# Kernel optimization log

Measured on AMD Instinct MI355X. Metric: run time of the kernel, lower is better.

The kernel has to match this reference:

```python
import jax, jax.numpy as jnp
import numpy as np

RATIOS = (0.5, 1.0, 2.0)
SCALES = (8.0, 16.0, 32.0)
BASE = 7.0
FEAT = 16
N_PRE = 6000    # pre-NMS top-k (test-mode default of standard ProposalCreator)
N_POST = 300    # post-NMS proposals per image (fixed -> jit-safe padded output)
NMS_T = 0.7
MIN_SIZE = 16.0
SCALE = 1.0     # forward arg `scale` default
NA = 9          # len(ratios)*len(anchor_scales)


def anchor_base():
    ab = np.zeros((NA, 4), np.float32)
    for i, r in enumerate(RATIOS):
        for j, s in enumerate(SCALES):
            h = BASE * s * np.sqrt(r)
            w = BASE * s * np.sqrt(1.0 / r)
            k = i * len(SCALES) + j
            ab[k] = [BASE / 2 - h / 2, BASE / 2 - w / 2, BASE / 2 + h / 2, BASE / 2 + w / 2]
    return jnp.asarray(ab)


def enum_anchors(H, W):
    # positions-major ordering: (H*W, 9, 4) -> (H*W*9, 4), matching permute(0,2,3,1)
    ab = anchor_base()
    sy = jnp.arange(H, dtype=jnp.float32) * FEAT
    sx = jnp.arange(W, dtype=jnp.float32) * FEAT
    ys, xs = jnp.meshgrid(sy, sx, indexing='ij')
    shift = jnp.stack([ys.ravel(), xs.ravel(), ys.ravel(), xs.ravel()], axis=1)
    return (shift[:, None, :] + ab[None, :, :]).reshape(-1, 4)


def conv2d(x, w, b, pad):
    y = jax.lax.conv_general_dilated(x, w, (1, 1), pad,
                                     dimension_numbers=('NCHW', 'OIHW', 'NCHW'))
    return y + b[None, :, None, None]


def decode(anchors, loc):
    ah = anchors[:, 2] - anchors[:, 0]
    aw = anchors[:, 3] - anchors[:, 1]
    acy = anchors[:, 0] + 0.5 * ah
    acx = anchors[:, 1] + 0.5 * aw
    dy, dx, dh, dw = loc[:, 0], loc[:, 1], loc[:, 2], loc[:, 3]
    cy = dy * ah + acy
    cx = dx * aw + acx
    h = jnp.exp(dh) * ah
    w = jnp.exp(dw) * aw
    return jnp.stack([cy - 0.5 * h, cx - 0.5 * w, cy + 0.5 * h, cx + 0.5 * w], axis=1)


def iou_matrix(b):
    tl = jnp.maximum(b[:, None, :2], b[None, :, :2])
    br = jnp.minimum(b[:, None, 2:], b[None, :, 2:])
    inter = jnp.prod(jnp.clip(br - tl, 0.0, None), axis=-1)
    area = jnp.prod(b[:, 2:] - b[:, :2], axis=-1)
    return inter / (area[:, None] + area[None, :] - inter + 1e-9)


def propose(loc, fg, anchors, img_h, img_w):
    boxes = decode(anchors, loc)
    boxes = jnp.stack([jnp.clip(boxes[:, 0], 0.0, img_h),
                       jnp.clip(boxes[:, 1], 0.0, img_w),
                       jnp.clip(boxes[:, 2], 0.0, img_h),
                       jnp.clip(boxes[:, 3], 0.0, img_w)], axis=1)
    hs = boxes[:, 2] - boxes[:, 0]
    ws = boxes[:, 3] - boxes[:, 1]
    ms = MIN_SIZE * SCALE
    valid = (hs >= ms) & (ws >= ms)
    score = jnp.where(valid, fg, -jnp.inf)
    _, idx = jax.lax.top_k(score, N_PRE)          # sorted by score desc
    bk = boxes[idx]                                # [N_PRE, 4]
    iou = iou_matrix(bk)                           # [N_PRE, N_PRE]

    def body(suppr, xs):
        row, i = xs
        keep_i = jnp.logical_not(suppr[i])
        suppr = suppr | (keep_i & (row > NMS_T) & (jnp.arange(N_PRE) > i))
        return suppr, None

    suppr, _ = jax.lax.scan(body, jnp.zeros(N_PRE, bool), (iou, jnp.arange(N_PRE)))
    keep = jnp.logical_not(suppr)
    # kept boxes first (already score-ordered), padded with trailing boxes
    sel = jnp.argsort(jnp.where(keep, jnp.arange(N_PRE), N_PRE))[:N_POST]
    return bk[sel]


def setup_inputs():
    key = jax.random.key(0)
    ks = jax.random.split(key, 4)
    N, C, H, W = 8, 256, 64, 64
    mid = 256
    return {
        'x': jax.random.normal(ks[0], (N, C, H, W), jnp.float32),
        'conv1_w': jax.random.normal(ks[1], (mid, C, 3, 3), jnp.float32) * 0.02,
        'conv1_b': jnp.zeros((mid,), jnp.float32),
        'score_w': jax.random.normal(ks[2], (NA * 2, mid, 1, 1), jnp.float32) * 0.02,
        'score_b': jnp.zeros((NA * 2,), jnp.float32),
        'loc_w': jax.random.normal(ks[3], (NA * 4, mid, 1, 1), jnp.float32) * 0.02,
        'loc_b': jnp.zeros((NA * 4,), jnp.float32),
        'img_h': 1024,
        'img_w': 1024,
    }


def reference(x, conv1_w, conv1_b, score_w, score_b, loc_w, loc_b, img_h, img_w):
    N, _, H, W = x.shape
    h = jax.nn.relu(conv2d(x, conv1_w, conv1_b, 'SAME'))
    rpn_loc = conv2d(h, loc_w, loc_b, 'VALID')
    rpn_score = conv2d(h, score_w, score_b, 'VALID')
    anchors = enum_anchors(H, W)                                 # [H*W*9, 4]
    rpn_loc = rpn_loc.transpose(0, 2, 3, 1).reshape(N, -1, 4)    # [N, A, 4]
    rpn_score = rpn_score.transpose(0, 2, 3, 1)                  # [N, H, W, 18]
    sm = jax.nn.softmax(rpn_score.reshape(N, H, W, NA, 2), axis=-1)
    fg = sm[..., 1].reshape(N, -1)                               # [N, A]
    rpn_score = rpn_score.reshape(N, -1, 2)
    fh, fw = float(img_h), float(img_w)
    rois = jax.lax.map(lambda a: propose(a[0], a[1], anchors, fh, fw),
                       (rpn_loc, fg)).reshape(-1, 4)             # [N*N_POST, 4]
    roi_indices = jnp.repeat(jnp.arange(N), N_POST)
    return rpn_loc, rpn_score, rois, roi_indices, anchors
```

## Files before the change

kernel.cpp:

```cpp
#include <hip/hip_runtime.h>
#include <cstdint>
#include <cstddef>

#define NBATCH 8
#define MID 256
#define HIMG 64
#define WIMG 64
#define NA 9
#define NPRE 6000
#define NPOST 300
#define NANCH (HIMG*WIMG*NA)
#define NWORDS 94
#define GCOLS 6016
#define LOROWS 16

#define OUT_LOC   0
#define OUT_SCORE 1179648
#define OUT_ROIS  1769472
#define OUT_RIDX  1779072
#define OUT_ANCH  1781472

#define H_OFF    0ul
#define H_BYTES  (8ul*256*64*64*4)
#define WT_OFF   (H_OFF + H_BYTES)
#define WT_BYTES (2304ul*256*4)
#define BOX_OFF  (WT_OFF + WT_BYTES)
#define BOX_BYTES (8ul*36864*4*4)
#define U_OFF    (BOX_OFF + BOX_BYTES)
#define U_BYTES  (8ul*36864*4)
#define CK_OFF   (U_OFF + U_BYTES)
#define CK_BYTES (8ul*8192*8)
#define CC_OFF   (CK_OFF + CK_BYTES)
#define CC_BYTES 64ul
#define BK_OFF   (CC_OFF + CC_BYTES)
#define BK_BYTES (8ul*6000*16)
#define M_OFF    (BK_OFF + BK_BYTES + 64)
#define M_BYTES  (8ul*NWORDS*GCOLS*8)

typedef _Float16 f16x8 __attribute__((ext_vector_type(8)));
typedef _Float16 f16x4 __attribute__((ext_vector_type(4)));
typedef float f32x16 __attribute__((ext_vector_type(16)));

__global__ __launch_bounds__(256) void k_prep_w(const float* __restrict__ w,
                                                const float* __restrict__ loc_w,
                                                const float* __restrict__ score_w,
                                                _Float16* __restrict__ w3h,
                                                _Float16* __restrict__ w3l,
                                                _Float16* __restrict__ whh,
                                                _Float16* __restrict__ whl,
                                                float* __restrict__ out,
                                                unsigned int* __restrict__ cc) {
    int idx = blockIdx.x * 256 + threadIdx.x;
    if (idx < 16) cc[idx] = 0u;
    if (idx < 589824) {
        int e  = idx & 7;
        int t  = idx >> 3;
        int oc = t & 255; t >>= 8;
        int g  = t & 1;   t >>= 1;
        int kb = t & 15;  t >>= 4;
        int s  = t;
        int ic = kb * 16 + g * 8 + e;
        float v = w[(oc * 256 + ic) * 9 + s] * 64.0f;
        _Float16 vh = (_Float16)v;
        w3h[idx] = vh;
        w3l[idx] = (_Float16)(v - (float)vh);
    } else if (idx < 589824 + 16384) {
        int j = idx - 589824;
        int e  = j & 7;
        int c  = (j >> 3) & 63;
        int g  = (j >> 9) & 1;
        int kb = j >> 10;
        int k  = kb * 16 + g * 8 + e;
        float v = (c < 36) ? loc_w[c * 256 + k]
                 : ((c < 54) ? score_w[(c - 36) * 256 + k] : 0.0f);
        v *= 64.0f;
        _Float16 vh = (_Float16)v;
        whh[j] = vh;
        whl[j] = (_Float16)(v - (float)vh);
    }
    if (idx < NANCH) {
        int p = idx / 9, a = idx - p * 9;
        int y = p >> 6, xg = p & 63;
        double rr = (a < 3) ? 0.5 : ((a < 6) ? 1.0 : 2.0);
        int sj = a % 3;
        double ssc = (sj == 0) ? 8.0 : ((sj == 1) ? 16.0 : 32.0);
        double hh = 7.0 * ssc * sqrt(rr);
        double ww = 7.0 * ssc * sqrt(1.0 / rr);
        float a0 = (float)(3.5 - 0.5 * hh), a2 = (float)(3.5 + 0.5 * hh);
        float b0 = (float)(3.5 - 0.5 * ww), b2 = (float)(3.5 + 0.5 * ww);
        float* dst = out + OUT_ANCH + (size_t)idx * 4;
        dst[0] = y * 16.0f + a0;
        dst[1] = xg * 16.0f + b0;
        dst[2] = y * 16.0f + a2;
        dst[3] = xg * 16.0f + b2;
    }
}

__global__ __launch_bounds__(1024) void k_conv1m(const float* __restrict__ x,
                                                 const _Float16* __restrict__ w3h,
                                                 const _Float16* __restrict__ w3l,
                                                 const float* __restrict__ bias,
                                                 float* __restrict__ h) {
    __shared__ __align__(16) _Float16 bt0[4 * 66 * 26];
    __shared__ __align__(16) _Float16 bt1[4 * 66 * 26];
    __shared__ float bsh[256];

    const int tid = threadIdx.x;
    const int lane = tid & 63;
    const int wv = tid >> 6;
    const int ocg = wv >> 1;
    const int wn = wv & 1;
    const int y0 = blockIdx.x * 2;
    const int n  = blockIdx.y;
    const int bl31 = lane & 31;
    const int g = lane >> 5;

    for (int i = tid; i < 858; i += 1024) {
        ((f16x8*)bt0)[i] = (f16x8){};
        ((f16x8*)bt1)[i] = (f16x8){};
    }
    if (tid < 256) bsh[tid] = bias[tid];

    f32x16 acc[2];
#pragma unroll
    for (int j = 0; j < 2; ++j)
#pragma unroll
        for (int e = 0; e < 16; ++e) acc[j][e] = 0.0f;

    const int scol = lane;
    const int sr   = wv & 3;
    const int sg   = wv >> 2;
    const int sgy  = y0 - 1 + sr;
    const bool gyok = (sgy >= 0) && (sgy < 64);
    const float* xrow = x + (size_t)n * 1048576 + sgy * 64 + scol;
    const int bto = (sr * 66 + scol + 1) * 26 + sg * 4;

    const int aoffl = (g * 256 + ocg * 32 + bl31) * 8;
    const _Float16* wph = w3h + aoffl;
    const _Float16* wpl = w3l + aoffl;

    float xr[4];
#pragma unroll
    for (int q = 0; q < 4; ++q)
        xr[q] = gyok ? xrow[(size_t)(sg * 4 + q) * 4096] : 0.0f;

    f16x8 AhC = *(const f16x8*)(wph);
    f16x8 AlC = *(const f16x8*)(wpl);

    for (int kb = 0; kb < 16; ++kb) {
        __syncthreads();
        {
            f16x4 hh, hl;
#pragma unroll
            for (int q = 0; q < 4; ++q) {
                float v = xr[q] * 64.0f;
                _Float16 vh = (_Float16)v;
                hh[q] = vh;
                hl[q] = (_Float16)(v - (float)vh);
            }
            *(f16x4*)&bt0[bto] = hh;
            *(f16x4*)&bt1[bto] = hl;
        }
        __syncthreads();
        if (kb < 15) {
#pragma unroll
            for (int q = 0; q < 4; ++q)
                xr[q] = gyok ? xrow[(size_t)((kb + 1) * 16 + sg * 4 + q) * 4096] : 0.0f;
        }

        const int ent00 = wn * 66 + bl31;
        f16x8 Bh0C = *(const f16x8*)&bt0[ent00 * 26 + g * 8];
        f16x8 Bl0C = *(const f16x8*)&bt1[ent00 * 26 + g * 8];
        f16x8 Bh1C = *(const f16x8*)&bt0[(ent00 + 32) * 26 + g * 8];
        f16x8 Bl1C = *(const f16x8*)&bt1[(ent00 + 32) * 26 + g * 8];

        const int kbn_base = (kb < 15) ? (kb + 1) : 15;
#pragma unroll
        for (int s = 0; s < 9; ++s) {
            const int sn  = (s == 8) ? 0 : (s + 1);
            const int kbn = (s == 8) ? kbn_base : kb;
            const _Float16* phn = wph + (size_t)kbn * 4096 + (size_t)sn * 65536;
            const _Float16* pln = wpl + (size_t)kbn * 4096 + (size_t)sn * 65536;
            f16x8 AhN = *(const f16x8*)(phn);
            f16x8 AlN = *(const f16x8*)(pln);

            f16x8 Bh0N = Bh0C, Bl0N = Bl0C, Bh1N = Bh1C, Bl1N = Bl1C;
            if (s < 8) {
                const int dyn = sn / 3 - 1, dxn = sn % 3 - 1;
                const int entn = (wn + dyn + 1) * 66 + dxn + 1 + bl31;
                const int en0 = entn * 26 + g * 8;
                const int en1 = (entn + 32) * 26 + g * 8;
                Bh0N = *(const f16x8*)&bt0[en0];
                Bl0N = *(const f16x8*)&bt1[en0];
                Bh1N = *(const f16x8*)&bt0[en1];
                Bl1N = *(const f16x8*)&bt1[en1];
            }

            __builtin_amdgcn_s_setprio(1);
            acc[0] = __builtin_amdgcn_mfma_f32_32x32x16_f16(AhC, Bh0C, acc[0], 0, 0, 0);
            acc[1] = __builtin_amdgcn_mfma_f32_32x32x16_f16(AhC, Bh1C, acc[1], 0, 0, 0);
            acc[0] = __builtin_amdgcn_mfma_f32_32x32x16_f16(AhC, Bl0C, acc[0], 0, 0, 0);
            acc[1] = __builtin_amdgcn_mfma_f32_32x32x16_f16(AhC, Bl1C, acc[1], 0, 0, 0);
            acc[0] = __builtin_amdgcn_mfma_f32_32x32x16_f16(AlC, Bh0C, acc[0], 0, 0, 0);
            acc[1] = __builtin_amdgcn_mfma_f32_32x32x16_f16(AlC, Bh1C, acc[1], 0, 0, 0);
            __builtin_amdgcn_s_setprio(0);

            AhC = AhN; AlC = AlN;
            Bh0C = Bh0N; Bl0C = Bl0N; Bh1C = Bh1N; Bl1C = Bl1N;
        }
    }

    const int colw = lane & 31;
    const int rgh = (lane >> 5) * 4;
    float* hn = h + (size_t)n * 1048576 + (size_t)(y0 + wn) * 64;
#pragma unroll
    for (int pcb = 0; pcb < 2; ++pcb)
#pragma unroll
        for (int reg = 0; reg < 16; ++reg) {
            const int row = (reg & 3) + 8 * (reg >> 2) + rgh;
            const int oc = ocg * 32 + row;
            float v = acc[pcb][reg] * 2.44140625e-4f + bsh[oc];
            hn[(size_t)oc * 4096 + pcb * 32 + colw] = fmaxf(v, 0.0f);
        }
}

__global__ __launch_bounds__(256) void k_headsm(const float* __restrict__ h,
                                                const _Float16* __restrict__ whh,
                                                const _Float16* __restrict__ whl,
                                                const float* __restrict__ loc_b,
                                                const float* __restrict__ score_b,
                                                const int* __restrict__ ihp,
                                                const int* __restrict__ iwp,
                                                float* __restrict__ out,
                                                float* __restrict__ boxes,
                                                unsigned int* __restrict__ ubuf) {
    __shared__ __align__(16) _Float16 bt0[128 * 18];
    __shared__ __align__(16) _Float16 bt1[128 * 18];
    __shared__ float outb[128 * 57];
    __shared__ float bsh[54];
    const int tid = threadIdx.x;
    const int lane = tid & 63;
    const int wv = tid >> 6;
    const int wm = wv >> 1;
    const int wpx = wv & 1;
    const int ptile = blockIdx.x;
    const int n = blockIdx.y;
    const int pxbase = ptile * 128;
    const int bl31 = lane & 31;
    const int g = lane >> 5;

    if (tid < 54) bsh[tid] = (tid < 36) ? loc_b[tid] : score_b[tid - 36];

    f32x16 acc[2];
#pragma unroll
    for (int j = 0; j < 2; ++j)
#pragma unroll
        for (int e = 0; e < 16; ++e) acc[j][e] = 0.0f;

    const int spx = tid >> 1;
    const int skg = (tid & 1) * 8;
    const float* hp = h + (size_t)n * 1048576 + pxbase + spx;
    const int aoff = (g * 64 + wm * 32 + bl31) * 8;

    for (int kb = 0; kb < 16; ++kb) {
        __syncthreads();
        {
            f16x8 hh, hl;
#pragma unroll
            for (int q = 0; q < 8; ++q) {
                float v = hp[(size_t)(kb * 16 + skg + q) * 4096] * 64.0f;
                _Float16 vh = (_Float16)v;
                hh[q] = vh;
                hl[q] = (_Float16)(v - (float)vh);
            }
            *(f16x8*)&bt0[spx * 18 + skg] = hh;
            *(f16x8*)&bt1[spx * 18 + skg] = hl;
        }
        __syncthreads();
        const _Float16* ph = whh + kb * 1024 + aoff;
        const _Float16* pl = whl + kb * 1024 + aoff;
        f16x8 Ah = *(const f16x8*)ph;
        f16x8 Al = *(const f16x8*)pl;
#pragma unroll
        for (int j = 0; j < 2; ++j) {
            const int px = wpx * 64 + j * 32 + bl31;
            f16x8 Bh = *(const f16x8*)&bt0[px * 18 + g * 8];
            f16x8 Bl = *(const f16x8*)&bt1[px * 18 + g * 8];
            acc[j] = __builtin_amdgcn_mfma_f32_32x32x16_f16(Ah, Bh, acc[j], 0, 0, 0);
            acc[j] = __builtin_amdgcn_mfma_f32_32x32x16_f16(Ah, Bl, acc[j], 0, 0, 0);
            acc[j] = __builtin_amdgcn_mfma_f32_32x32x16_f16(Al, Bh, acc[j], 0, 0, 0);
        }
    }

#pragma unroll
    for (int j = 0; j < 2; ++j)
#pragma unroll
        for (int reg = 0; reg < 16; ++reg) {
            const int row = (reg & 3) + 8 * (reg >> 2) + (g << 2);
            const int c = wm * 32 + row;
            if (c < 54) {
                const int px = wpx * 64 + j * 32 + bl31;
                outb[px * 57 + c] = acc[j][reg] * 2.44140625e-4f + bsh[c];
            }
        }
    __syncthreads();

    const float fh = (float)(*ihp), fwid = (float)(*iwp);
    for (int slot = tid; slot < 128 * 9; slot += 256) {
        int pli = slot / 9, a = slot - pli * 9;
        int p = ptile * 128 + pli;
        int y = p >> 6, xg = p & 63;
        float l0 = outb[pli * 57 + a * 4 + 0];
        float l1 = outb[pli * 57 + a * 4 + 1];
        float l2 = outb[pli * 57 + a * 4 + 2];
        float l3 = outb[pli * 57 + a * 4 + 3];
        float s0 = outb[pli * 57 + 36 + a * 2 + 0];
        float s1 = outb[pli * 57 + 36 + a * 2 + 1];
        size_t base = (size_t)n * NANCH + (size_t)p * 9 + a;
        ((float4*)(out + OUT_LOC))[base] = make_float4(l0, l1, l2, l3);
        ((float2*)(out + OUT_SCORE))[base] = make_float2(s0, s1);
        float mx = fmaxf(s0, s1);
        float e0 = expf(s0 - mx), e1 = expf(s1 - mx);
        float fg = e1 / (e0 + e1);
        double rr = (a < 3) ? 0.5 : ((a < 6) ? 1.0 : 2.0);
        int sj = a % 3;
        double ssc = (sj == 0) ? 8.0 : ((sj == 1) ? 16.0 : 32.0);
        double hhd = 7.0 * ssc * sqrt(rr);
        double wwd = 7.0 * ssc * sqrt(1.0 / rr);
        float a0 = (float)(3.5 - 0.5 * hhd), a2 = (float)(3.5 + 0.5 * hhd);
        float b0 = (float)(3.5 - 0.5 * wwd), b2 = (float)(3.5 + 0.5 * wwd);
        float ay1 = y * 16.0f + a0, ay2 = y * 16.0f + a2;
        float ax1 = xg * 16.0f + b0, ax2 = xg * 16.0f + b2;
        float ah = ay2 - ay1, aw = ax2 - ax1;
        float acy = ay1 + 0.5f * ah, acx = ax1 + 0.5f * aw;
        float cy = l0 * ah + acy, cx = l1 * aw + acx;
        float bh = expf(l2) * ah, bw = expf(l3) * aw;
        float y1 = fminf(fmaxf(cy - 0.5f * bh, 0.f), fh);
        float x1 = fminf(fmaxf(cx - 0.5f * bw, 0.f), fwid);
        float y2 = fminf(fmaxf(cy + 0.5f * bh, 0.f), fh);
        float x2 = fminf(fmaxf(cx + 0.5f * bw, 0.f), fwid);
        ((float4*)boxes)[base] = make_float4(y1, x1, y2, x2);
        bool valid = ((y2 - y1) >= 16.0f) && ((x2 - x1) >= 16.0f);
        float sc = valid ? fg : -__builtin_inff();
        unsigned int ub = __float_as_uint(sc);
        ub = (ub & 0x80000000u) ? ~ub : (ub | 0x80000000u);
        ubuf[base] = ub;
    }
}

__global__ __launch_bounds__(1024) void k_select(const unsigned int* __restrict__ ubuf,
                                                 unsigned long long* __restrict__ ckeys,
                                                 unsigned int* __restrict__ cc) {
    __shared__ unsigned int hist[256];
    __shared__ unsigned int selb;
    __shared__ int rank_s;
    __shared__ unsigned int lcnt;
    const int tid = threadIdx.x;
    const int lane = tid & 63;
    const int b = blockIdx.x;
    const unsigned int* ub = ubuf + (size_t)b * NANCH;
    if (tid == 0) { rank_s = NPRE - 1; lcnt = 0; }
    unsigned int prefix = 0;
    for (int pass = 0; pass < 4; ++pass) {
        int shift = 24 - 8 * pass;
        if (tid < 256) hist[tid] = 0;
        __syncthreads();
        for (int i = tid; i < NANCH; i += 1024) {
            unsigned int u = ub[i];
            bool ok = (pass == 0) || ((u >> (shift + 8)) == (prefix >> (shift + 8)));
            unsigned int byt = (u >> shift) & 255u;
            if (pass == 0) {
                unsigned long long todo = __ballot(ok);
                while (todo) {
                    int src = __builtin_ctzll(todo);
                    unsigned int bb = __shfl(byt, src, 64);
                    unsigned long long m = __ballot(ok && (byt == bb));
                    if (lane == src) atomicAdd(&hist[bb], (unsigned int)__popcll(m));
                    todo &= ~m;
                }
            } else {
                if (ok) atomicAdd(&hist[byt], 1u);
            }
        }
        __syncthreads();
        const int r = rank_s;
        for (int off = 1; off < 256; off <<= 1) {
            unsigned int v = 0;
            if (tid < 256 && tid + off < 256) v = hist[tid + off];
            __syncthreads();
            if (tid < 256) hist[tid] += v;
            __syncthreads();
        }
        if (tid < 256) {
            unsigned int inc = hist[tid];
            unsigned int above = (tid == 255) ? 0u : hist[tid + 1];
            if ((int)inc > r && (int)above <= r) {
                selb = (unsigned int)tid;
                rank_s = r - (int)above;
            }
        }
        __syncthreads();
        prefix |= (selb << shift);
        __syncthreads();
    }
    const unsigned int ustar = prefix;
    for (int i = tid; i < NANCH; i += 1024) {
        unsigned int u = ub[i];
        bool sel2 = (u >= ustar);
        unsigned long long m = __ballot(sel2);
        if (m) {
            int src = __builtin_ctzll(m);
            unsigned int base2 = 0;
            if (lane == src) base2 = atomicAdd(&lcnt, (unsigned int)__popcll(m));
            base2 = __shfl(base2, src, 64);
            if (sel2) {
                unsigned int pos = base2 + (unsigned int)__popcll(m & ((1ull << lane) - 1ull));
                if (pos < 8192)
                    ckeys[(size_t)b * 8192 + pos] =
                        ((unsigned long long)u << 32) | (unsigned int)(0xFFFFFFFFu - (unsigned int)i);
            }
        }
    }
    __syncthreads();
    if (tid == 0) cc[b] = (lcnt > 8192u) ? 8192u : lcnt;
}

__device__ __forceinline__ void cswap_u64(unsigned long long& a, unsigned long long& c, bool desc) {
    bool sw = desc ? (a < c) : (a > c);
    unsigned long long t0 = sw ? c : a;
    unsigned long long t1 = sw ? a : c;
    a = t0; c = t1;
}
__device__ __forceinline__ void net8(unsigned long long v[8], bool d) {
    cswap_u64(v[0], v[4], d); cswap_u64(v[1], v[5], d); cswap_u64(v[2], v[6], d); cswap_u64(v[3], v[7], d);
    cswap_u64(v[0], v[2], d); cswap_u64(v[1], v[3], d); cswap_u64(v[4], v[6], d); cswap_u64(v[5], v[7], d);
    cswap_u64(v[0], v[1], d); cswap_u64(v[2], v[3], d); cswap_u64(v[4], v[5], d); cswap_u64(v[6], v[7], d);
}
__device__ __forceinline__ unsigned long long shfl_xor_u64(unsigned long long x, int lmask) {
    unsigned int lo = (unsigned int)x, hi = (unsigned int)(x >> 32);
    lo = __shfl_xor(lo, lmask, 64);
    hi = __shfl_xor(hi, lmask, 64);
    return ((unsigned long long)hi << 32) | lo;
}

__global__ __launch_bounds__(256) void k_sort_loc(unsigned long long* __restrict__ ckeys,
                                                  const unsigned int* __restrict__ cc) {
    __shared__ unsigned long long S[2048];
    const int tid = threadIdx.x;
    const int seg = blockIdx.x;
    const int b = blockIdx.y;
    const int cnt = (int)cc[b];
    const int gbase = seg * 2048 + tid * 8;
    const int lb = tid * 8;
    unsigned long long* ck = ckeys + (size_t)b * 8192;

    unsigned long long v[8];
#pragma unroll
    for (int e = 0; e < 8; ++e) {
        int i = gbase + e;
        v[e] = (i < cnt) ? ck[i] : 0ull;
    }
    cswap_u64(v[0], v[1], true);  cswap_u64(v[2], v[3], false);
    cswap_u64(v[4], v[5], true);  cswap_u64(v[6], v[7], false);
    cswap_u64(v[0], v[2], true);  cswap_u64(v[1], v[3], true);
    cswap_u64(v[4], v[6], false); cswap_u64(v[5], v[7], false);
    cswap_u64(v[0], v[1], true);  cswap_u64(v[2], v[3], true);
    cswap_u64(v[4], v[5], false); cswap_u64(v[6], v[7], false);
    net8(v, (gbase & 8) == 0);

    for (int k = 16; k <= 2048; k <<= 1) {
        for (int j = k >> 1; j >= 8; j >>= 1) {
            const bool keep_max = (((gbase & k) == 0) != ((gbase & j) != 0));
            if (j >= 512) {
                __syncthreads();
#pragma unroll
                for (int e = 0; e < 8; ++e) S[lb + e] = v[e];
                __syncthreads();
                const int pb = lb ^ j;
#pragma unroll
                for (int e = 0; e < 8; ++e) {
                    unsigned long long p = S[pb + e];
                    v[e] = keep_max ? (v[e] >= p ? v[e] : p) : (v[e] <= p ? v[e] : p);
                }
            } else {
                const int lmask = j >> 3;
#pragma unroll
                for (int e = 0; e < 8; ++e) {
                    unsigned long long p = shfl_xor_u64(v[e], lmask);
                    v[e] = keep_max ? (v[e] >= p ? v[e] : p) : (v[e] <= p ? v[e] : p);
                }
            }
        }
        net8(v, (gbase & k) == 0);
    }
#pragma unroll
    for (int e = 0; e < 8; ++e) ck[gbase + e] = v[e];
}

__global__ __launch_bounds__(256) void k_sort_gmerge(unsigned long long* __restrict__ ckeys,
                                                     int j, int k) {
    const int t = blockIdx.x * 256 + threadIdx.x;
    const int b = blockIdx.y;
    const int i = ((t & ~(j - 1)) << 1) | (t & (j - 1));
    const int l = i | j;
    unsigned long long* ck = ckeys + (size_t)b * 8192;
    unsigned long long a = ck[i], c = ck[l];
    const bool desc = ((i & k) == 0);
    bool sw = desc ? (a < c) : (a > c);
    if (sw) { ck[i] = c; ck[l] = a; }
}

__global__ __launch_bounds__(256) void k_sort_tail(unsigned long long* __restrict__ ckeys,
                                                   int k,
                                                   const float* __restrict__ boxes,
                                                   float* __restrict__ bk,
                                                   int dogather) {
    __shared__ unsigned long long S[2048];
    const int tid = threadIdx.x;
    const int seg = blockIdx.x;
    const int b = blockIdx.y;
    const int gbase = seg * 2048 + tid * 8;
    const int lb = tid * 8;
    unsigned long long* ck = ckeys + (size_t)b * 8192;

    unsigned long long v[8];
#pragma unroll
    for (int e = 0; e < 8; ++e) v[e] = ck[gbase + e];

    for (int j = 1024; j >= 8; j >>= 1) {
        const bool keep_max = (((gbase & k) == 0) != ((gbase & j) != 0));
        if (j >= 512) {
            __syncthreads();
#pragma unroll
            for (int e = 0; e < 8; ++e) S[lb + e] = v[e];
            __syncthreads();
            const int pb = lb ^ j;
#pragma unroll
            for (int e = 0; e < 8; ++e) {
                unsigned long long p = S[pb + e];
                v[e] = keep_max ? (v[e] >= p ? v[e] : p) : (v[e] <= p ? v[e] : p);
            }
        } else {
            const int lmask = j >> 3;
#pragma unroll
            for (int e = 0; e < 8; ++e) {
                unsigned long long p = shfl_xor_u64(v[e], lmask);
                v[e] = keep_max ? (v[e] >= p ? v[e] : p) : (v[e] <= p ? v[e] : p);
            }
        }
    }
    net8(v, (gbase & k) == 0);

    if (!dogather) {
#pragma unroll
        for (int e = 0; e < 8; ++e) ck[gbase + e] = v[e];
    } else {
#pragma unroll
        for (int e = 0; e < 8; ++e) {
            int i = gbase + e;
            if (i < NPRE) {
                unsigned int idx = 0xFFFFFFFFu - (unsigned int)(v[e] & 0xFFFFFFFFull);
                if (idx >= NANCH) idx = NANCH - 1;
                float4 bx = ((const float4*)boxes)[(size_t)b * NANCH + idx];
                ((float4*)bk)[(size_t)b * NPRE + i] = bx;
            }
        }
    }
}

__global__ __launch_bounds__(256) void k_mask(const float* __restrict__ bk,
                                              unsigned long long* __restrict__ MT,
                                              const unsigned int* __restrict__ cc,
                                              int iwbase, int checkdone) {
    const int iw = iwbase + blockIdx.x;
    const int gb = blockIdx.y;
    const int b = blockIdx.z;
    if (checkdone && cc[8 + b] != 0u) return;
    if (iw > 4 * gb + 3) return;
    const int tid = threadIdx.x;
    __shared__ float4 jb[64];
    __shared__ float ja[64];
    if (tid < 64) {
        int j = iw * 64 + tid;
        float4 v = (j < NPRE) ? ((const float4*)bk)[(size_t)b * NPRE + j]
                              : make_float4(0.f, 0.f, 0.f, 0.f);
        jb[tid] = v;
        ja[tid] = (v.z - v.x) * (v.w - v.y);
    }
    __syncthreads();
    const int g = gb * 256 + tid;
    float4 bi = (g < NPRE) ? ((const float4*)bk)[(size_t)b * NPRE + g]
                           : make_float4(0.f, 0.f, 0.f, 0.f);
    float ai = (bi.z - bi.x) * (bi.w - bi.y);
    const double MD = (double)0.7f + 0x1p-25;
    unsigned long long word = 0ull;
#pragma unroll 8
    for (int jj = 0; jj < 64; ++jj) {
        float4 bj = jb[jj];
        float aj = ja[jj];
        float ty = fmaxf(bi.x, bj.x), tx = fmaxf(bi.y, bj.y);
        float by = fminf(bi.z, bj.z), bx = fminf(bi.w, bj.w);
        float ihh = fmaxf(by - ty, 0.f), iww = fmaxf(bx - tx, 0.f);
        float inter = ihh * iww;
        float den = ai + aj - inter + 1e-9f;
        if ((double)inter >= MD * (double)den) word |= (1ull << jj);
    }
    if (g < GCOLS)
        MT[((size_t)b * NWORDS + iw) * GCOLS + g] = word;
}

__global__ __launch_bounds__(1024) void k_nms_try(const unsigned long long* __restrict__ MT,
                                                  const float* __restrict__ bk,
                                                  float* __restrict__ out,
                                                  unsigned int* __restrict__ cc) {
    const int b = blockIdx.x;
    const int tid = threadIdx.x;
    const int lane = tid & 63;
    __shared__ unsigned long long keptw[NWORDS];
    __shared__ unsigned long long dead[LOROWS];
    __shared__ int sel[NPOST];
    __shared__ int totkept;
    const unsigned long long* mtb = MT + (size_t)b * NWORDS * GCOLS;

    for (int i = tid; i < NWORDS; i += 1024) keptw[i] = 0ull;
    if (tid < LOROWS) dead[tid] = 0ull;
    if (tid == 0) totkept = 0;
    __syncthreads();

    for (int c = 0; c < LOROWS; ++c) {
        if (tid < 64) {
            const int g = c * 64 + lane;
            unsigned long long diag = mtb[(size_t)c * GCOLS + g];
            bool deadl = (((dead[c] >> lane) & 1ull) != 0ull) || (g >= NPRE);
            unsigned long long undec = ~__ballot(deadl);
            unsigned long long kc = 0ull;
            while (undec) {
                int i = __builtin_ctzll(undec);
                kc |= (1ull << i);
                unsigned long long supm = __ballot((diag >> i) & 1ull);
                undec &= ~(supm | (1ull << i));
            }
            if (lane == 0) { keptw[c] = kc; totkept += __popcll(kc); }
        }
        __syncthreads();
        if (totkept >= NPOST) break;
        const unsigned long long kc = keptw[c];
        if (kc) {
            for (int g2 = (c + 1) * 64 + tid; g2 < LOROWS * 64; g2 += 1024) {
                unsigned long long w = mtb[(size_t)c * GCOLS + g2] & kc;
                unsigned long long m = __ballot(w != 0ull);
                if (lane == 0 && m) atomicOr(&dead[g2 >> 6], m);
            }
        }
        __syncthreads();
    }

    const int done = (totkept >= NPOST) ? 1 : 0;
    if (tid == 0) cc[8 + b] = (unsigned int)done;
    if (!done) return;

    if (tid == 0) {
        int pos = 0;
        for (int w = 0; w < NWORDS && pos < NPOST; ++w) {
            unsigned long long kw = keptw[w];
            while (kw && pos < NPOST) {
                int i2 = __builtin_ctzll(kw);
                sel[pos++] = w * 64 + i2;
                kw &= kw - 1;
            }
        }
    }
    __syncthreads();
    for (int s2 = tid; s2 < NPOST; s2 += 1024) {
        int i = sel[s2];
        float4 bx = ((const float4*)bk)[(size_t)b * NPRE + i];
        ((float4*)(out + OUT_ROIS))[b * NPOST + s2] = bx;
        out[OUT_RIDX + b * NPOST + s2] = (float)b;
    }
}

__global__ __launch_bounds__(1024) void k_nms_full(const unsigned long long* __restrict__ MT,
                                                   const float* __restrict__ bk,
                                                   float* __restrict__ out,
                                                   const unsigned int* __restrict__ cc) {
    const int b = blockIdx.x;
    if (cc[8 + b] != 0u) return;
    const int tid = threadIdx.x;
    const int lane = tid & 63;
    __shared__ unsigned long long keptw[NWORDS];
    __shared__ unsigned long long dead[NWORDS];
    __shared__ int sel[NPOST];
    __shared__ int totkept;
    const unsigned long long* mtb = MT + (size_t)b * NWORDS * GCOLS;

    for (int i = tid; i < NWORDS; i += 1024) { dead[i] = 0ull; keptw[i] = 0ull; }
    if (tid == 0) totkept = 0;
    __syncthreads();

    for (int c = 0; c < NWORDS; ++c) {
        if (tid < 64) {
            const int g = c * 64 + lane;
            unsigned long long diag = mtb[(size_t)c * GCOLS + g];
            bool deadl = (((dead[c] >> lane) & 1ull) != 0ull) || (g >= NPRE);
            unsigned long long undec = ~__ballot(deadl);
            unsigned long long kc = 0ull;
            while (undec) {
                int i = __builtin_ctzll(undec);
                kc |= (1ull << i);
                unsigned long long supm = __ballot((diag >> i) & 1ull);
                undec &= ~(supm | (1ull << i));
            }
            if (lane == 0) { keptw[c] = kc; totkept += __popcll(kc); }
        }
        __syncthreads();
        if (totkept >= NPOST) break;
        const unsigned long long kc = keptw[c];
        if (kc) {
            for (int g2 = (c + 1) * 64 + tid; g2 < GCOLS; g2 += 1024) {
                unsigned long long w = mtb[(size_t)c * GCOLS + g2] & kc;
                unsigned long long m = __ballot(w != 0ull);
                if (lane == 0 && m) atomicOr(&dead[g2 >> 6], m);
            }
        }
        __syncthreads();
    }

    if (tid == 0) {
        int pos = 0;
        for (int w = 0; w < NWORDS && pos < NPOST; ++w) {
            unsigned long long kw = keptw[w];
            while (kw && pos < NPOST) {
                int i2 = __builtin_ctzll(kw);
                sel[pos++] = w * 64 + i2;
                kw &= kw - 1;
            }
        }
        for (int w = 0; w < NWORDS && pos < NPOST; ++w) {
            int nvalid = NPRE - w * 64; if (nvalid > 64) nvalid = 64;
            unsigned long long vm = (nvalid >= 64) ? ~0ull : ((1ull << nvalid) - 1ull);
            unsigned long long sw = (~keptw[w]) & vm;
            while (sw && pos < NPOST) {
                int i2 = __builtin_ctzll(sw);
                sel[pos++] = w * 64 + i2;
                sw &= sw - 1;
            }
        }
    }
    __syncthreads();
    for (int s2 = tid; s2 < NPOST; s2 += 1024) {
        int i = sel[s2];
        float4 bx = ((const float4*)bk)[(size_t)b * NPRE + i];
        ((float4*)(out + OUT_ROIS))[b * NPOST + s2] = bx;
        out[OUT_RIDX + b * NPOST + s2] = (float)b;
    }
}

extern "C" void kernel_launch(void* const* d_in, const int* in_sizes, int n_in,
                              void* d_out, int out_size, void* d_ws, size_t ws_size,
                              hipStream_t stream) {
    const float* x = (const float*)d_in[0];
    const float* conv1_w = (const float*)d_in[1];
    const float* conv1_b = (const float*)d_in[2];
    const float* score_w = (const float*)d_in[3];
    const float* score_b = (const float*)d_in[4];
    const float* loc_w = (const float*)d_in[5];
    const float* loc_b = (const float*)d_in[6];
    const int* ihp = (const int*)d_in[7];
    const int* iwp = (const int*)d_in[8];
    float* out = (float*)d_out;
    char* ws = (char*)d_ws;
    float* h = (float*)(ws + H_OFF);
    _Float16* w3h = (_Float16*)(ws + WT_OFF);
    _Float16* w3l = (_Float16*)(ws + WT_OFF + 1179648ul);
    float* boxes = (float*)(ws + BOX_OFF);
    unsigned int* ubuf = (unsigned int*)(ws + U_OFF);
    unsigned long long* ckeys = (unsigned long long*)(ws + CK_OFF);
    unsigned int* cc = (unsigned int*)(ws + CC_OFF);
    float* bk = (float*)(ws + BK_OFF);
    unsigned long long* MT = (unsigned long long*)(ws + M_OFF);
    _Float16* whh = (_Float16*)(ws + CK_OFF);
    _Float16* whl = (_Float16*)(ws + CK_OFF + 32768ul);

    hipLaunchKernelGGL(k_prep_w, dim3(2368), dim3(256), 0, stream,
                       conv1_w, loc_w, score_w, w3h, w3l, whh, whl, out, cc);
    hipLaunchKernelGGL(k_conv1m, dim3(32, 8), dim3(1024), 0, stream, x, w3h, w3l, conv1_b, h);
    hipLaunchKernelGGL(k_headsm, dim3(32, 8), dim3(256), 0, stream,
                       h, whh, whl, loc_b, score_b, ihp, iwp, out, boxes, ubuf);
    hipLaunchKernelGGL(k_select, dim3(8), dim3(1024), 0, stream, ubuf, ckeys, cc);
    hipLaunchKernelGGL(k_sort_loc, dim3(4, 8), dim3(256), 0, stream, ckeys, cc);
    hipLaunchKernelGGL(k_sort_gmerge, dim3(16, 8), dim3(256), 0, stream, ckeys, 2048, 4096);
    hipLaunchKernelGGL(k_sort_tail, dim3(4, 8), dim3(256), 0, stream, ckeys, 4096, boxes, bk, 0);
    hipLaunchKernelGGL(k_sort_gmerge, dim3(16, 8), dim3(256), 0, stream, ckeys, 4096, 8192);
    hipLaunchKernelGGL(k_sort_gmerge, dim3(16, 8), dim3(256), 0, stream, ckeys, 2048, 8192);
    hipLaunchKernelGGL(k_sort_tail, dim3(4, 8), dim3(256), 0, stream, ckeys, 8192, boxes, bk, 1);
    hipLaunchKernelGGL(k_mask, dim3(LOROWS, 24, 8), dim3(256), 0, stream, bk, MT, cc, 0, 0);
    hipLaunchKernelGGL(k_nms_try, dim3(8), dim3(1024), 0, stream, MT, bk, out, cc);
    hipLaunchKernelGGL(k_mask, dim3(NWORDS - LOROWS, 24, 8), dim3(256), 0, stream, bk, MT, cc, LOROWS, 1);
    hipLaunchKernelGGL(k_nms_full, dim3(8), dim3(1024), 0, stream, MT, bk, out, cc);
}
```

Baseline: 400.1 us.

## Fuse 1x1 head convs into conv1 kernel, dropping intermediate h buffer

Merges the head kernel into the 3x3 conv kernel. Each block now converts its relu'd conv1 accumulators straight into fp16 hi/lo tiles in shared memory and runs the 1x1 loc/score MFMA inside the same block, with the two K halves split across waves and then reduced. This removes the 32 MB fp32 write and read of the intermediate feature map and one kernel launch. In exchange it adds many block-level barriers, and the decode tail now runs with only 1152 slots over 1024 threads.

```diff
diff --git a/kernel.cpp b/kernel.cpp
--- a/kernel.cpp
+++ b/kernel.cpp
@@ -100,10 +100,23 @@
                                                  const _Float16* __restrict__ w3h,
                                                  const _Float16* __restrict__ w3l,
                                                  const float* __restrict__ bias,
-                                                 float* __restrict__ h) {
-    __shared__ __align__(16) _Float16 bt0[4 * 66 * 26];
-    __shared__ __align__(16) _Float16 bt1[4 * 66 * 26];
+                                                 const _Float16* __restrict__ whh,
+                                                 const _Float16* __restrict__ whl,
+                                                 const float* __restrict__ loc_b,
+                                                 const float* __restrict__ score_b,
+                                                 const int* __restrict__ ihp,
+                                                 const int* __restrict__ iwp,
+                                                 float* __restrict__ out,
+                                                 float* __restrict__ boxes,
+                                                 unsigned int* __restrict__ ubuf) {
+    __shared__ __align__(16) char smem[38656];
     __shared__ float bsh[256];
+    _Float16* bt0 = (_Float16*)smem;
+    _Float16* bt1 = (_Float16*)(smem + 13728);
+    _Float16* hb0 = (_Float16*)smem;
+    _Float16* hb1 = (_Float16*)(smem + 4608);
+    float*    outb = (float*)(smem + 9216);
+    float*    bsh2 = (float*)(smem + 38400);
 
     const int tid = threadIdx.x;
     const int lane = tid & 63;
@@ -114,6 +127,7 @@
     const int n  = blockIdx.y;
     const int bl31 = lane & 31;
     const int g = lane >> 5;
+    const int rgh = g * 4;
 
     for (int i = tid; i < 858; i += 1024) {
         ((f16x8*)bt0)[i] = (f16x8){};
@@ -210,103 +224,82 @@
         }
     }
 
-    const int colw = lane & 31;
-    const int rgh = (lane >> 5) * 4;
-    float* hn = h + (size_t)n * 1048576 + (size_t)(y0 + wn) * 64;
-#pragma unroll
-    for (int pcb = 0; pcb < 2; ++pcb)
+    __syncthreads();
+    if (tid < 54) bsh2[tid] = (tid < 36) ? loc_b[tid] : score_b[tid - 36];
+
+    const int khalf = wv & 1;
+    const int cm    = (wv >> 1) & 1;
+    const int pxt   = wv >> 2;
+    const int haoff = (g * 64 + cm * 32 + bl31) * 8;
+    const int colw  = bl31;
+
+    f32x16 hacc;
+#pragma unroll
+    for (int e = 0; e < 16; ++e) hacc[e] = 0.0f;
+
+#pragma unroll
+    for (int kb = 0; kb < 16; ++kb) {
+        if ((kb >> 1) == ocg) {
+            const int rh = (kb & 1) * 8;
+#pragma unroll
+            for (int ridx = 0; ridx < 8; ++ridx) {
+                const int reg = rh + ridx;
+                const int row = (reg & 3) + 8 * (reg >> 2) + rgh;
+                const int kk = row & 15;
+                const float bv = bsh[ocg * 32 + row];
+#pragma unroll
+                for (int pcb = 0; pcb < 2; ++pcb) {
+                    float v = fmaxf(acc[pcb][reg] * 2.44140625e-4f + bv, 0.0f);
+                    float hv = v * 64.0f;
+                    _Float16 vh = (_Float16)hv;
+                    const int px = wn * 64 + pcb * 32 + colw;
+                    hb0[px * 18 + kk] = vh;
+                    hb1[px * 18 + kk] = (_Float16)(hv - (float)vh);
+                }
+            }
+        }
+        __syncthreads();
+        if ((kb & 1) == khalf) {
+            const _Float16* ph = whh + kb * 1024 + haoff;
+            const _Float16* pl = whl + kb * 1024 + haoff;
+            f16x8 Ah = *(const f16x8*)ph;
+            f16x8 Al = *(const f16x8*)pl;
+            const int hpx = pxt * 32 + bl31;
+            f16x8 Bh = *(const f16x8*)&hb0[hpx * 18 + g * 8];
+            f16x8 Bl = *(const f16x8*)&hb1[hpx * 18 + g * 8];
+            hacc = __builtin_amdgcn_mfma_f32_32x32x16_f16(Ah, Bh, hacc, 0, 0, 0);
+            hacc = __builtin_amdgcn_mfma_f32_32x32x16_f16(Ah, Bl, hacc, 0, 0, 0);
+            hacc = __builtin_amdgcn_mfma_f32_32x32x16_f16(Al, Bh, hacc, 0, 0, 0);
+        }
+        __syncthreads();
+    }
+
+    if (khalf == 1) {
 #pragma unroll
         for (int reg = 0; reg < 16; ++reg) {
             const int row = (reg & 3) + 8 * (reg >> 2) + rgh;
-            const int oc = ocg * 32 + row;
-            float v = acc[pcb][reg] * 2.44140625e-4f + bsh[oc];
-            hn[(size_t)oc * 4096 + pcb * 32 + colw] = fmaxf(v, 0.0f);
-        }
-}
-
-__global__ __launch_bounds__(256) void k_headsm(const float* __restrict__ h,
-                                                const _Float16* __restrict__ whh,
-                                                const _Float16* __restrict__ whl,
-                                                const float* __restrict__ loc_b,
-                                                const float* __restrict__ score_b,
-                                                const int* __restrict__ ihp,
-                                                const int* __restrict__ iwp,
-                                                float* __restrict__ out,
-                                                float* __restrict__ boxes,
-                                                unsigned int* __restrict__ ubuf) {
-    __shared__ __align__(16) _Float16 bt0[128 * 18];
-    __shared__ __align__(16) _Float16 bt1[128 * 18];
-    __shared__ float outb[128 * 57];
-    __shared__ float bsh[54];
-    const int tid = threadIdx.x;
-    const int lane = tid & 63;
-    const int wv = tid >> 6;
-    const int wm = wv >> 1;
-    const int wpx = wv & 1;
+            const int c = cm * 32 + row;
+            if (c < 54)
+                outb[(pxt * 32 + colw) * 57 + c] = hacc[reg] * 2.44140625e-4f;
+        }
+    }
+    __syncthreads();
+    if (khalf == 0) {
+#pragma unroll
+        for (int reg = 0; reg < 16; ++reg) {
+            const int row = (reg & 3) + 8 * (reg >> 2) + rgh;
+            const int c = cm * 32 + row;
+            if (c < 54) {
+                const int o = (pxt * 32 + colw) * 57 + c;
+                outb[o] = hacc[reg] * 2.44140625e-4f + bsh2[c] + outb[o];
+            }
+        }
+    }
+    __syncthreads();
+
     const int ptile = blockIdx.x;
-    const int n = blockIdx.y;
-    const int pxbase = ptile * 128;
-    const int bl31 = lane & 31;
-    const int g = lane >> 5;
-
-    if (tid < 54) bsh[tid] = (tid < 36) ? loc_b[tid] : score_b[tid - 36];
-
-    f32x16 acc[2];
-#pragma unroll
-    for (int j = 0; j < 2; ++j)
-#pragma unroll
-        for (int e = 0; e < 16; ++e) acc[j][e] = 0.0f;
-
-    const int spx = tid >> 1;
-    const int skg = (tid & 1) * 8;
-    const float* hp = h + (size_t)n * 1048576 + pxbase + spx;
-    const int aoff = (g * 64 + wm * 32 + bl31) * 8;
-
-    for (int kb = 0; kb < 16; ++kb) {
-        __syncthreads();
-        {
-            f16x8 hh, hl;
-#pragma unroll
-            for (int q = 0; q < 8; ++q) {
-                float v = hp[(size_t)(kb * 16 + skg + q) * 4096] * 64.0f;
-                _Float16 vh = (_Float16)v;
-                hh[q] = vh;
-                hl[q] = (_Float16)(v - (float)vh);
-            }
-            *(f16x8*)&bt0[spx * 18 + skg] = hh;
-            *(f16x8*)&bt1[spx * 18 + skg] = hl;
-        }
-        __syncthreads();
-        const _Float16* ph = whh + kb * 1024 + aoff;
-        const _Float16* pl = whl + kb * 1024 + aoff;
-        f16x8 Ah = *(const f16x8*)ph;
-        f16x8 Al = *(const f16x8*)pl;
-#pragma unroll
-        for (int j = 0; j < 2; ++j) {
-            const int px = wpx * 64 + j * 32 + bl31;
-            f16x8 Bh = *(const f16x8*)&bt0[px * 18 + g * 8];
-            f16x8 Bl = *(const f16x8*)&bt1[px * 18 + g * 8];
-            acc[j] = __builtin_amdgcn_mfma_f32_32x32x16_f16(Ah, Bh, acc[j], 0, 0, 0);
-            acc[j] = __builtin_amdgcn_mfma_f32_32x32x16_f16(Ah, Bl, acc[j], 0, 0, 0);
-            acc[j] = __builtin_amdgcn_mfma_f32_32x32x16_f16(Al, Bh, acc[j], 0, 0, 0);
-        }
-    }
-
-#pragma unroll
-    for (int j = 0; j < 2; ++j)
-#pragma unroll
-        for (int reg = 0; reg < 16; ++reg) {
-            const int row = (reg & 3) + 8 * (reg >> 2) + (g << 2);
-            const int c = wm * 32 + row;
-            if (c < 54) {
-                const int px = wpx * 64 + j * 32 + bl31;
-                outb[px * 57 + c] = acc[j][reg] * 2.44140625e-4f + bsh[c];
-            }
-        }
-    __syncthreads();
-
     const float fh = (float)(*ihp), fwid = (float)(*iwp);
-    for (int slot = tid; slot < 128 * 9; slot += 256) {
+    for (int slot = tid; slot < 128 * 9; slot += 1024) {
         int pli = slot / 9, a = slot - pli * 9;
         int p = ptile * 128 + pli;
         int y = p >> 6, xg = p & 63;
@@ -769,7 +762,6 @@
     const int* iwp = (const int*)d_in[8];
     float* out = (float*)d_out;
     char* ws = (char*)d_ws;
-    float* h = (float*)(ws + H_OFF);
     _Float16* w3h = (_Float16*)(ws + WT_OFF);
     _Float16* w3l = (_Float16*)(ws + WT_OFF + 1179648ul);
     float* boxes = (float*)(ws + BOX_OFF);
@@ -783,9 +775,9 @@
 
     hipLaunchKernelGGL(k_prep_w, dim3(2368), dim3(256), 0, stream,
                        conv1_w, loc_w, score_w, w3h, w3l, whh, whl, out, cc);
-    hipLaunchKernelGGL(k_conv1m, dim3(32, 8), dim3(1024), 0, stream, x, w3h, w3l, conv1_b, h);
-    hipLaunchKernelGGL(k_headsm, dim3(32, 8), dim3(256), 0, stream,
-                       h, whh, whl, loc_b, score_b, ihp, iwp, out, boxes, ubuf);
+    hipLaunchKernelGGL(k_conv1m, dim3(32, 8), dim3(1024), 0, stream,
+                       x, w3h, w3l, conv1_b, whh, whl, loc_b, score_b, ihp, iwp,
+                       out, boxes, ubuf);
     hipLaunchKernelGGL(k_select, dim3(8), dim3(1024), 0, stream, ubuf, ckeys, cc);
     hipLaunchKernelGGL(k_sort_loc, dim3(4, 8), dim3(256), 0, stream, ckeys, cc);
     hipLaunchKernelGGL(k_sort_gmerge, dim3(16, 8), dim3(256), 0, stream, ckeys, 2048, 4096);
```

Result: slower. 547.5 us (+36.9%).
